# Optimization experiments

Measured on AMD Instinct MI355X. Metric: run time of the kernel, lower is better.

Reference implementation:

```python
import jax, jax.numpy as jnp
import numpy as np

H, C, PQ, PV, CZ, CS = 12, 16, 4, 8, 128, 384
W_C = (2.0 / (9.0 * PQ)) ** 0.5
INV_SQRT3 = 3.0 ** -0.5


def setup_inputs() -> dict:
    key = jax.random.key(0)
    ks = jax.random.split(key, 20)
    B, N = 2, 512
    s = jax.random.normal(ks[0], (B, N, CS), jnp.float32)
    z = jax.random.normal(ks[1], (B, N, N, CZ), jnp.float32)
    m = jax.random.normal(ks[2], (B, N, 3, 3), jnp.float32)
    rot, _ = jnp.linalg.qr(m)  # proper-ish rotations (orthonormal frames)
    trans = jax.random.normal(ks[3], (B, N, 3), jnp.float32)
    seq_mask = jnp.ones((B, N), jnp.float32)
    sc = 0.02
    params = {
        'Wq': jax.random.normal(ks[4], (CS, H * C)) * sc,
        'bq': jnp.zeros((H * C,)),
        'Wkv': jax.random.normal(ks[5], (CS, H * C * 2)) * sc,
        'bkv': jnp.zeros((H * C * 2,)),
        'Wb': jax.random.normal(ks[6], (CZ, H)) * sc,
        'bb': jnp.zeros((H,)),
        'Wqp': jax.random.normal(ks[7], (CS, 3 * PQ * H)) * sc,
        'bqp': jnp.zeros((3 * PQ * H,)),
        'Wkvp': jax.random.normal(ks[8], (CS, 3 * (PQ + PV) * H)) * sc,
        'bkvp': jnp.zeros((3 * (PQ + PV) * H,)),
        'gamma': jnp.zeros((H,)),
        'Wout': jax.random.normal(ks[9], ((CZ + C + PV * 4) * H, CS)) * sc,
        'bout': jnp.zeros((CS,)),
    }
    return dict(s=s, z=z, rot=rot, trans=trans, seq_mask=seq_mask, **params)


def reference(s, z, rot, trans, seq_mask, Wq, bq, Wkv, bkv, Wb, bb, Wqp, bqp, Wkvp, bkvp, gamma, Wout, bout):
    B, N, _ = s.shape
    # scalar q/k/v
    q = (s @ Wq + bq).reshape(B, N, H, C)
    kv = (s @ Wkv + bkv).reshape(B, N, H, 2 * C)
    k, v = kv[..., :C], kv[..., C:]
    qp = s @ Wqp + bqp                                   # (B,N,3*PQ*H)
    qp = jnp.stack(jnp.split(qp, 3, axis=-1), axis=-1)   # (B,N,PQ*H,3)
    qp = jnp.einsum('bixy,bipy->bipx', rot, qp) + trans[:, :, None, :]
    qp = qp.reshape(B, N, H, PQ, 3)
    # key/value points
    kvp = s @ Wkvp + bkvp
    kvp = jnp.stack(jnp.split(kvp, 3, axis=-1), axis=-1)  # (B,N,(PQ+PV)*H,3)
    kvp = jnp.einsum('bixy,bipy->bipx', rot, kvp) + trans[:, :, None, :]
    kvp = kvp.reshape(B, N, H, PQ + PV, 3)
    kp, vp = kvp[..., :PQ, :], kvp[..., PQ:, :]
    # attention logits: scalar term + pair bias + point-distance term
    bpair = (z @ Wb + bb).transpose(0, 3, 1, 2)          # (B,H,i,j)
    a = jnp.einsum('bihc,bjhc->bhij', q, k) * (3 * C) ** -0.5 + INV_SQRT3 * bpair
    d2 = jnp.sum((qp[:, :, None] - kp[:, None]) ** 2, axis=-1)   # (B,i,j,H,PQ)
    pa = -0.5 * jnp.sum(d2, axis=-1)                      # (B,i,j,H)
    head_w = jax.nn.softplus(gamma)
    pa = pa * (head_w * W_C * INV_SQRT3)
    a = a + pa.transpose(0, 3, 1, 2)
    mask_bias = 100000.0 * (seq_mask[:, :, None] * seq_mask[:, None, :] - 1.0)
    a = a + mask_bias[:, None, :, :]
    a = jax.nn.softmax(a, axis=-1)                        # (B,H,i,j)
    # outputs: scalar values, rotated points (inverse frame), pair features
    o = jnp.einsum('bhij,bjhc->bihc', a, v).reshape(B, N, H * C)
    op = jnp.einsum('bhij,bjhpx->bihpx', a, vp)           # (B,i,H,PV,3)
    op = jnp.einsum('biyx,bihpy->bihpx', rot, op - trans[:, :, None, None, :])  # R^T(p-t)
    onorm = jnp.maximum(jnp.sqrt(jnp.sum(op ** 2, axis=-1)), 1e-6).reshape(B, N, H * PV)
    op = op.reshape(B, N, H * PV, 3)
    opair = jnp.einsum('bhij,bijc->bihc', a, z).reshape(B, N, H * CZ)
    feat = jnp.concatenate([o, op[..., 0], op[..., 1], op[..., 2], onorm, opair], axis=-1)
    return feat @ Wout + bout
```

## Files before the change

### kernel.cpp

```cpp
#include <hip/hip_runtime.h>
#include <hip/hip_bf16.h>

constexpr int B = 2, N = 512, H = 12, C = 16, PQ = 4, PV = 8, CZ = 128, CS = 384;
constexpr int HC   = H * C;
constexpr int FEAT = (CZ + C + PV * 4) * H;
constexpr float QK_SCALE  = 0.14433756729740643f;
constexpr float INV_SQRT3 = 0.5773502691896258f;
constexpr float WC_IS3    = 0.13608276348795434f;

using f32x4 = __attribute__((ext_vector_type(4))) float;
using s16x8 = __attribute__((ext_vector_type(8))) short;

__device__ __forceinline__ short f2b(float f) {
    union { __hip_bfloat16 b; short s; } u;
    u.b = __float2bfloat16(f);
    return u.s;
}
__device__ __forceinline__ float b2f(short s) {
    union { short s; __hip_bfloat16 b; } u;
    u.s = s;
    return __bfloat162float(u.b);
}

constexpr int RPB = 2;

__global__ __launch_bounds__(256) void k_proj(
    const float* __restrict__ s, const float* __restrict__ rot, const float* __restrict__ trans,
    const float* __restrict__ Wq, const float* __restrict__ bq,
    const float* __restrict__ Wkv, const float* __restrict__ bkv,
    const float* __restrict__ Wqp, const float* __restrict__ bqp,
    const float* __restrict__ Wkvp, const float* __restrict__ bkvp,
    const float* __restrict__ gamma, const float* __restrict__ bb,
    const float* __restrict__ Wout,
    short* __restrict__ qcw, short* __restrict__ kkp,
    float* __restrict__ vw, float* __restrict__ vpw,
    short* __restrict__ pcw, float* __restrict__ auxw,
    short* __restrict__ WT)
{
    __shared__ float s_s[RPB][CS];
    __shared__ float rawqp_s[RPB][144];
    __shared__ float rawkvp_s[RPB][432];
    __shared__ float qrot_s[RPB][48][3];
    __shared__ float sq_s[RPB][48];
    __shared__ float R_s[RPB][9], T_s[RPB][3];
    const int t = threadIdx.x;
    const int bi0 = blockIdx.x * RPB;

    for (int idx = t; idx < RPB * CS / 4; idx += 256) {
        int r = idx / (CS / 4), k4 = idx % (CS / 4);
        ((float4*)s_s[r])[k4] = ((const float4*)(s + (size_t)(bi0 + r) * CS))[k4];
    }
    if (t < RPB * 9) R_s[t / 9][t % 9] = rot[bi0 * 9 + t];
    if (t < RPB * 3) T_s[t / 3][t % 3] = trans[bi0 * 3 + t];
    __syncthreads();

    for (int qd = t; qd < 288; qd += 256) {
        const int c = qd * 4;
        const float* Wp; int ldw; const float* bp;
        int seg;
        if (c < 192)      { Wp = Wq   + c;        ldw = 192; bp = bq + c;        seg = 0; }
        else if (c < 576) { Wp = Wkv  + (c - 192); ldw = 384; bp = bkv + (c - 192); seg = 1; }
        else if (c < 720) { Wp = Wqp  + (c - 576); ldw = 144; bp = bqp + (c - 576); seg = 2; }
        else              { Wp = Wkvp + (c - 720); ldw = 432; bp = bkvp + (c - 720); seg = 3; }
        float4 bv = *(const float4*)bp;
        float acc[RPB][4];
        #pragma unroll
        for (int r = 0; r < RPB; ++r) {
            acc[r][0] = bv.x; acc[r][1] = bv.y; acc[r][2] = bv.z; acc[r][3] = bv.w;
        }
        for (int k4 = 0; k4 < CS / 4; ++k4) {
            float4 sv[RPB];
            #pragma unroll
            for (int r = 0; r < RPB; ++r) sv[r] = *(const float4*)&s_s[r][k4 * 4];
            #pragma unroll
            for (int e = 0; e < 4; ++e) {
                float4 wv = *(const float4*)(Wp + (size_t)(k4 * 4 + e) * ldw);
                #pragma unroll
                for (int r = 0; r < RPB; ++r) {
                    float se = ((const float*)&sv[r])[e];
                    acc[r][0] += se * wv.x; acc[r][1] += se * wv.y;
                    acc[r][2] += se * wv.z; acc[r][3] += se * wv.w;
                }
            }
        }
        if (seg == 0) {
            #pragma unroll
            for (int r = 0; r < RPB; ++r) {
                short4 o = make_short4(f2b(QK_SCALE * acc[r][0]), f2b(QK_SCALE * acc[r][1]),
                                       f2b(QK_SCALE * acc[r][2]), f2b(QK_SCALE * acc[r][3]));
                *(short4*)&qcw[(size_t)(bi0 + r) * 192 + c] = o;
            }
        } else if (seg == 1) {
            int cc = c - 192, h = cc >> 5, w5 = cc & 31;
            if (w5 < 16) {
                #pragma unroll
                for (int r = 0; r < RPB; ++r) {
                    short4 o = make_short4(f2b(acc[r][0]), f2b(acc[r][1]),
                                           f2b(acc[r][2]), f2b(acc[r][3]));
                    *(short4*)&kkp[(size_t)(bi0 + r) * 384 + h * 16 + w5] = o;
                }
            } else {
                #pragma unroll
                for (int r = 0; r < RPB; ++r) {
                    int row = bi0 + r;
                    *(float4*)&vw[(size_t)row * 192 + h * 16 + (w5 - 16)] =
                        (float4){acc[r][0], acc[r][1], acc[r][2], acc[r][3]};
                }
            }
        } else if (seg == 2) {
            #pragma unroll
            for (int r = 0; r < RPB; ++r)
                *(float4*)&rawqp_s[r][c - 576] = (float4){acc[r][0], acc[r][1], acc[r][2], acc[r][3]};
        } else {
            #pragma unroll
            for (int r = 0; r < RPB; ++r)
                *(float4*)&rawkvp_s[r][c - 720] = (float4){acc[r][0], acc[r][1], acc[r][2], acc[r][3]};
        }
    }
    __syncthreads();

    for (int idx = t; idx < RPB * 48; idx += 256) {
        int r = idx / 48, p = idx % 48;
        float y0 = rawqp_s[r][p], y1 = rawqp_s[r][48 + p], y2 = rawqp_s[r][96 + p];
        #pragma unroll
        for (int x = 0; x < 3; ++x)
            qrot_s[r][p][x] = T_s[r][x] + R_s[r][x * 3] * y0 + R_s[r][x * 3 + 1] * y1 + R_s[r][x * 3 + 2] * y2;
    }
    for (int idx = t; idx < RPB * 144; idx += 256) {
        int r = idx / 144, p = idx % 144, h = p / 12, pp = p % 12;
        float y0 = rawkvp_s[r][p], y1 = rawkvp_s[r][144 + p], y2 = rawkvp_s[r][288 + p];
        float vals[3]; float ss = 0.0f;
        #pragma unroll
        for (int x = 0; x < 3; ++x) {
            float v = T_s[r][x] + R_s[r][x * 3] * y0 + R_s[r][x * 3 + 1] * y1 + R_s[r][x * 3 + 2] * y2;
            vals[x] = v; ss += v * v;
        }
        int row = bi0 + r;
        if (pp < PQ) {
            #pragma unroll
            for (int x = 0; x < 3; ++x)
                kkp[(size_t)row * 384 + 192 + h * 16 + pp * 3 + x] = f2b(vals[x]);
            sq_s[r][h * 4 + pp] = ss;
        } else {
            #pragma unroll
            for (int x = 0; x < 3; ++x)
                vpw[(size_t)row * 288 + h * 24 + (pp - PQ) * 3 + x] = vals[x];
        }
    }
    __syncthreads();

    if (t < RPB * 12) {
        int r = t / 12, h = t % 12, row = bi0 + r;
        float g = gamma[h];
        float sp = fmaxf(g, 0.0f) + log1pf(expf(-fabsf(g)));
        float pac = -0.5f * sp * WC_IS3;
        float kpsq = sq_s[r][h * 4] + sq_s[r][h * 4 + 1] + sq_s[r][h * 4 + 2] + sq_s[r][h * 4 + 3];
        kkp[(size_t)row * 384 + 192 + h * 16 + 12] = f2b(kpsq);
        kkp[(size_t)row * 384 + 192 + h * 16 + 13] = 0;
        kkp[(size_t)row * 384 + 192 + h * 16 + 14] = 0;
        kkp[(size_t)row * 384 + 192 + h * 16 + 15] = 0;
        float qpsq = 0.0f;
        #pragma unroll
        for (int pq = 0; pq < 4; ++pq)
            #pragma unroll
            for (int x = 0; x < 3; ++x) {
                float qv = qrot_s[r][h * 4 + pq][x];
                qpsq += qv * qv;
                pcw[(size_t)row * 192 + h * 16 + pq * 3 + x] = f2b(-2.0f * pac * qv);
            }
        pcw[(size_t)row * 192 + h * 16 + 12] = f2b(pac);
        pcw[(size_t)row * 192 + h * 16 + 13] = 0;
        pcw[(size_t)row * 192 + h * 16 + 14] = 0;
        pcw[(size_t)row * 192 + h * 16 + 15] = 0;
        auxw[(size_t)row * 16 + h] = INV_SQRT3 * bb[h] + pac * qpsq;
    }
    if (t >= RPB * 12 && t < RPB * 16) {
        int r = (t - RPB * 12) >> 2, hh = 12 + ((t - RPB * 12) & 3);
        auxw[(size_t)(bi0 + r) * 16 + hh] = 0.0f;
    }

    short* tileb = (short*)&s_s[0][0];
    for (int tile = blockIdx.x; tile < 66 * 12; tile += 512) {
        const int k0 = (tile % 66) * 32;
        const int c0 = (tile / 66) * 32;
        __syncthreads();
        {
            int r = t >> 3, c4 = (t & 7) * 4;
            float4 v = *(const float4*)&Wout[(size_t)(k0 + r) * CS + c0 + c4];
            tileb[(c4 + 0) * 33 + r] = f2b(v.x);
            tileb[(c4 + 1) * 33 + r] = f2b(v.y);
            tileb[(c4 + 2) * 33 + r] = f2b(v.z);
            tileb[(c4 + 3) * 33 + r] = f2b(v.w);
        }
        __syncthreads();
        {
            int rr = t >> 3, k4 = (t & 7) * 4;
            short4 o = make_short4(tileb[rr * 33 + k4], tileb[rr * 33 + k4 + 1],
                                   tileb[rr * 33 + k4 + 2], tileb[rr * 33 + k4 + 3]);
            *(short4*)&WT[(size_t)(c0 + rr) * FEAT + k0 + k4] = o;
        }
    }
}

constexpr int PLS = 520;
constexpr int BSEL = 56;

#define LOADZ(BUF, PTR)                                                  \
    {                                                                    \
        _Pragma("unroll")                                                \
        for (int k4 = 0; k4 < 4; ++k4) {                                 \
            BUF[k4 * 2]     = *(const float4*)((PTR) + k4 * 32);         \
            BUF[k4 * 2 + 1] = *(const float4*)((PTR) + k4 * 32 + 4);     \
        }                                                                \
    }

#define COMPUTE(BUF, JC, KPTR)                                                     \
    {                                                                              \
        s16x8 zf[4];                                                               \
        _Pragma("unroll")                                                          \
        for (int kk = 0; kk < 4; ++kk) {                                           \
            float4 u0 = BUF[kk * 2], u1 = BUF[kk * 2 + 1];                         \
            s16x8 f;                                                               \
            f[0] = f2b(u0.x); f[1] = f2b(u0.y); f[2] = f2b(u0.z); f[3] = f2b(u0.w);\
            f[4] = f2b(u1.x); f[5] = f2b(u1.y); f[6] = f2b(u1.z); f[7] = f2b(u1.w);\
            zf[kk] = f;                                                            \
        }                                                                          \
        f32x4 accA = (f32x4){0, 0, 0, 0}, accB = (f32x4){0, 0, 0, 0};              \
        f32x4 accC = (f32x4){0, 0, 0, 0}, accD = (f32x4){0, 0, 0, 0};              \
        _Pragma("unroll")                                                          \
        for (int kk = 0; kk < 4; ++kk) {                                           \
            s16x8 wb = *(const s16x8*)(bl + kk * 8);                               \
            accA = __builtin_amdgcn_mfma_f32_16x16x32_bf16(zf[kk], wb, accA, 0, 0, 0);\
        }                                                                          \
        s16x8 qselr = *(const s16x8*)(bl + 32);                                    \
        s16x8 pselr = *(const s16x8*)(bl + 40);                                    \
        _Pragma("unroll")                                                          \
        for (int kk = 0; kk < 4; ++kk) {                                           \
            s16x8 af = *(const s16x8*)((KPTR) + kk * 32);                          \
            s16x8 bsel = (kk == half) ? qselr : z8;                                \
            accB = __builtin_amdgcn_mfma_f32_16x16x32_bf16(af, bsel, accB, 0, 0, 0); \
        }                                                                          \
        _Pragma("unroll")                                                          \
        for (int kk = 4; kk < 8; ++kk) {                                           \
            s16x8 af = *(const s16x8*)((KPTR) + kk * 32);                          \
            s16x8 bsel;                                                            \
            if (kk < 6) bsel = (kk == half) ? qselr : z8;                          \
            else        bsel = ((kk - 6) == half) ? pselr : z8;                    \
            accC = __builtin_amdgcn_mfma_f32_16x16x32_bf16(af, bsel, accC, 0, 0, 0); \
        }                                                                          \
        _Pragma("unroll")                                                          \
        for (int kk = 8; kk < 12; ++kk) {                                          \
            s16x8 af = *(const s16x8*)((KPTR) + kk * 32);                          \
            s16x8 bsel = ((kk - 6) == half) ? pselr : z8;                          \
            accD = __builtin_amdgcn_mfma_f32_16x16x32_bf16(af, bsel, accD, 0, 0, 0); \
        }                                                                          \
        f32x4 acc = (accA + accB) + (accC + accD);                                 \
        float4 m4 = *(const float4*)(mkp + (JC) * 16);                             \
        float lo[4]; float cm = -INFINITY;                                         \
        _Pragma("unroll")                                                          \
        for (int r = 0; r < 4; ++r) {                                              \
            lo[r] = acc[r] + constH + 100000.0f * (mask_i * ((const float*)&m4)[r] - 1.0f); \
            cm = fmaxf(cm, lo[r]);                                                 \
        }                                                                          \
        cm = fmaxf(cm, __shfl_xor(cm, 16, 64));                                    \
        cm = fmaxf(cm, __shfl_xor(cm, 32, 64));                                    \
        float mnew = fmaxf(m_run, cm);                                             \
        float sc = __expf(m_run - mnew);                                           \
        m_run = mnew;                                                              \
        float p[4]; float ps = 0.0f;                                               \
        _Pragma("unroll")                                                          \
        for (int r = 0; r < 4; ++r) { p[r] = __expf(lo[r] - mnew); ps += p[r]; }   \
        ps += __shfl_xor(ps, 16, 64);                                              \
        ps += __shfl_xor(ps, 32, 64);                                              \
        l_run = l_run * sc + ps;                                                   \
        if (sc != 1.0f) {                                                          \
            for (int jj = lg * 4; jj < (JC) * 16; jj += 16) {                      \
                short* pr = &P_lds[m15 * PLS + jw + jj];                           \
                _Pragma("unroll")                                                  \
                for (int r = 0; r < 4; ++r) pr[r] = f2b(b2f(pr[r]) * sc);          \
            }                                                                      \
        }                                                                          \
        *(short4*)&P_lds[m15 * PLS + jw + (JC) * 16 + lg * 4] =                    \
            make_short4(f2b(p[0]), f2b(p[1]), f2b(p[2]), f2b(p[3]));               \
    }

__global__ __launch_bounds__(256) void k_attn2(
    const float* __restrict__ z, const float* __restrict__ rot, const float* __restrict__ trans,
    const float* __restrict__ seq_mask,
    const float* __restrict__ Wb,
    const short* __restrict__ qcw, const short* __restrict__ kkp,
    const short* __restrict__ pcw, const float* __restrict__ auxw,
    const float* __restrict__ vw, const float* __restrict__ vpw,
    short* __restrict__ featb)
{
    __shared__ short P_lds[16 * PLS];
    __shared__ __align__(16) char ovl[7680];
    short* bsel_lds = (short*)ovl;
    float* ored_s   = (float*)ovl;
    float* opred_s  = (float*)(ovl + 3072);
    float* op_f     = (float*)(ovl + 6528);
    __shared__ float ml_s[4][16], ll_s[4][16], M_s[16], Linv_s[16];
    __shared__ float R_s[9], T_s[3];

    const int t = threadIdx.x;
    const int w   = t >> 6;
    const int l   = t & 63;
    const int lg  = l >> 4;
    const int m15 = l & 15;
    const int bi  = blockIdx.x;
    const int b   = bi >> 9;
    const int i   = bi & (N - 1);

    if (t < 9) R_s[t] = rot[bi * 9 + t];
    if (t < 3) T_s[t] = trans[bi * 3 + t];

    const bool hv = (m15 < 12);
    const int hcl = hv ? m15 : 0;
    const int half = m15 >> 1;
    const float constH = auxw[(size_t)bi * 16 + m15];
    const float mask_i = seq_mask[bi];

    if (w == 0) {
        short* dst = &bsel_lds[l * BSEL];
        #pragma unroll
        for (int kk = 0; kk < 4; ++kk)
            #pragma unroll
            for (int e = 0; e < 8; ++e) {
                int c = kk * 32 + lg * 8 + e;
                dst[kk * 8 + e] = f2b(hv ? INV_SQRT3 * Wb[c * H + hcl] : 0.0f);
            }
        const bool selh = ((lg >> 1) == (m15 & 1));
        const s16x8 z8v = {0, 0, 0, 0, 0, 0, 0, 0};
        const short* qrow = qcw + (size_t)bi * 192 + hcl * 16;
        s16x8 qlo = *(const s16x8*)qrow;
        s16x8 qhi = *(const s16x8*)(qrow + 8);
        s16x8 q = (hv && selh) ? ((lg & 1) ? qhi : qlo) : z8v;
        const short* prow = pcw + (size_t)bi * 192 + hcl * 16;
        s16x8 plo = *(const s16x8*)prow;
        s16x8 phi = *(const s16x8*)(prow + 8);
        s16x8 p = (hv && selh) ? ((lg & 1) ? phi : plo) : z8v;
        *(s16x8*)(dst + 32) = q;
        *(s16x8*)(dst + 40) = p;
    }
    __syncthreads();

    float m_run = -INFINITY, l_run = 0.0f;

    const size_t zbase = ((size_t)b * N + i) * (size_t)(N * CZ);
    const int jw = w * 128;
    const float* zAp = z + zbase + (size_t)(jw + m15) * CZ + lg * 8;
    const short* kAp = kkp + (size_t)(b * N + jw + m15) * 384 + lg * 8;
    const float* mkp = seq_mask + b * N + jw + lg * 4;
    const short* bl = &bsel_lds[l * BSEL];
    const s16x8 z8 = {0, 0, 0, 0, 0, 0, 0, 0};

    float4 bufA[8], bufB[8];
    LOADZ(bufA, zAp);

    for (int jc2 = 0; jc2 < 8; jc2 += 2) {
        LOADZ(bufB, zAp + 16 * CZ);
        COMPUTE(bufA, jc2, kAp);
        kAp += 6144;
        {
            const float* nx = zAp + ((jc2 == 6) ? (16 * CZ) : (32 * CZ));
            LOADZ(bufA, nx);
        }
        COMPUTE(bufB, jc2 + 1, kAp);
        kAp += 6144;
        zAp += 32 * CZ;
    }

    if (lg == 0) { ml_s[w][m15] = m_run; ll_s[w][m15] = l_run; }
    __syncthreads();
    if (t < 16) {
        float M = ml_s[0][t];
        M = fmaxf(M, ml_s[1][t]); M = fmaxf(M, ml_s[2][t]); M = fmaxf(M, ml_s[3][t]);
        float Lt = 0.0f;
        #pragma unroll
        for (int ww = 0; ww < 4; ++ww) Lt += ll_s[ww][t] * __expf(ml_s[ww][t] - M);
        M_s[t] = M;
        Linv_s[t] = 1.0f / Lt;
    }
    __syncthreads();

    {
        const int h = t >> 4, j0t = (t & 15) * 32;
        const int wv = j0t >> 7;
        const float sS = __expf(ml_s[wv][h] - M_s[h]) * Linv_s[h];
        #pragma unroll
        for (int k = 0; k < 4; ++k) {
            s16x8 v = *(const s16x8*)&P_lds[h * PLS + j0t + k * 8];
            s16x8 o;
            #pragma unroll
            for (int e = 0; e < 8; ++e) o[e] = f2b(b2f(v[e]) * sS);
            *(s16x8*)&P_lds[h * PLS + j0t + k * 8] = o;
        }
    }
    __syncthreads();

    short* F = featb + (size_t)bi * FEAT;

    f32x4 oa0 = (f32x4){0, 0, 0, 0}, oa1 = (f32x4){0, 0, 0, 0};
    const int c0 = w * 32;
    #pragma unroll 4
    for (int kk = 0; kk < 16; ++kk) {
        s16x8 af = *(const s16x8*)&P_lds[m15 * PLS + kk * 32 + lg * 8];
        const float* zb = z + zbase + (size_t)(kk * 32 + lg * 8) * CZ + c0 + m15;
        s16x8 b0f, b1f;
        #pragma unroll
        for (int e = 0; e < 8; ++e) {
            b0f[e] = f2b(zb[(size_t)e * CZ]);
            b1f[e] = f2b(zb[(size_t)e * CZ + 16]);
        }
        oa0 = __builtin_amdgcn_mfma_f32_16x16x32_bf16(af, b0f, oa0, 0, 0, 0);
        oa1 = __builtin_amdgcn_mfma_f32_16x16x32_bf16(af, b1f, oa1, 0, 0, 0);
    }
    #pragma unroll
    for (int r = 0; r < 4; ++r) {
        int h = lg * 4 + r;
        if (h < 12) {
            F[576 + h * 128 + c0 + m15]      = f2b(oa0[r]);
            F[576 + h * 128 + c0 + 16 + m15] = f2b(oa1[r]);
        }
    }

    if (t < 192) {
        const int c4 = t % 48, jg = t / 48;
        const int h = c4 >> 2;
        const short* Pr = &P_lds[h * PLS + jg * 128];
        const float* vb = vw + ((size_t)b * N + jg * 128) * 192 + c4 * 4;
        f32x4 a = (f32x4){0, 0, 0, 0};
        #pragma unroll 2
        for (int q = 0; q < 16; ++q) {
            s16x8 pv = *(const s16x8*)(Pr + q * 8);
            #pragma unroll
            for (int e = 0; e < 8; ++e) {
                float4 v4 = *(const float4*)(vb + (size_t)(q * 8 + e) * 192);
                float pj = b2f(pv[e]);
                a[0] += pj * v4.x; a[1] += pj * v4.y; a[2] += pj * v4.z; a[3] += pj * v4.w;
            }
        }
        *(f32x4*)&ored_s[jg * 192 + c4 * 4] = a;
    }

    if (t < 216) {
        const int c4 = t % 72, jg = t / 72;
        const int h = c4 / 6;
        const int j0g = (jg == 0) ? 0 : (jg == 1 ? 176 : 352);
        const int nq = (jg == 2) ? 20 : 22;
        const short* Pr = &P_lds[h * PLS + j0g];
        const float* vb = vpw + ((size_t)b * N + j0g) * 288 + c4 * 4;
        f32x4 a = (f32x4){0, 0, 0, 0};
        #pragma unroll 2
        for (int q = 0; q < nq; ++q) {
            s16x8 pv = *(const s16x8*)(Pr + q * 8);
            #pragma unroll
            for (int e = 0; e < 8; ++e) {
                float4 v4 = *(const float4*)(vb + (size_t)(q * 8 + e) * 288);
                float pj = b2f(pv[e]);
                a[0] += pj * v4.x; a[1] += pj * v4.y; a[2] += pj * v4.z; a[3] += pj * v4.w;
            }
        }
        *(f32x4*)&opred_s[jg * 288 + c4 * 4] = a;
    }
    __syncthreads();

    if (t < 192)
        F[t] = f2b(ored_s[t] + ored_s[192 + t] + ored_s[384 + t] + ored_s[576 + t]);
    if (t < 72) {
        #pragma unroll
        for (int x = 0; x < 4; ++x) {
            int rv = t * 4 + x;
            op_f[rv] = opred_s[rv] + opred_s[288 + rv] + opred_s[576 + rv];
        }
    }
    __syncthreads();

    if (t < 96) {
        float o0 = op_f[t * 3 + 0] - T_s[0];
        float o1 = op_f[t * 3 + 1] - T_s[1];
        float o2 = op_f[t * 3 + 2] - T_s[2];
        float n2 = 0.0f;
        #pragma unroll
        for (int x = 0; x < 3; ++x) {
            float rx = R_s[0 * 3 + x] * o0 + R_s[1 * 3 + x] * o1 + R_s[2 * 3 + x] * o2;
            F[HC + 96 * x + t] = f2b(rx);
            n2 += rx * rx;
        }
        F[480 + t] = f2b(fmaxf(sqrtf(n2), 1e-6f));
    }
}

__global__ __launch_bounds__(256) void k_out(
    const short* __restrict__ featb, const short* __restrict__ WT,
    const float* __restrict__ bout, float* __restrict__ out)
{
    __shared__ short A_s[32 * 40];
    __shared__ short B_s[64 * 40];
    const int t = threadIdx.x;
    const int w   = t >> 6;
    const int l   = t & 63;
    const int lg  = l >> 4;
    const int m15 = l & 15;
    const int wm = w >> 1, wn = w & 1;
    const int bm = (blockIdx.x / 6) * 32;
    const int bn = (blockIdx.x % 6) * 64;

    f32x4 acc[2];
    acc[0] = (f32x4){0, 0, 0, 0};
    acc[1] = (f32x4){0, 0, 0, 0};

    const int sr = t >> 2;
    const int sk = (t & 3) * 8;

    s16x8 rA, rB;
    if (t < 128) rA = *(const s16x8*)&featb[(size_t)(bm + sr) * FEAT + sk];
    rB = *(const s16x8*)&WT[(size_t)(bn + sr) * FEAT + sk];

    for (int k0 = 0; k0 < FEAT; k0 += 32) {
        __syncthreads();
        if (t < 128) *(s16x8*)&A_s[sr * 40 + sk] = rA;
        *(s16x8*)&B_s[sr * 40 + sk] = rB;
        __syncthreads();

        const int kn = k0 + 32;
        if (kn < FEAT) {
            if (t < 128) rA = *(const s16x8*)&featb[(size_t)(bm + sr) * FEAT + kn + sk];
            rB = *(const s16x8*)&WT[(size_t)(bn + sr) * FEAT + kn + sk];
        }

        s16x8 af = *(const s16x8*)&A_s[(wm * 16 + m15) * 40 + lg * 8];
        #pragma unroll
        for (int sn = 0; sn < 2; ++sn) {
            s16x8 bf = *(const s16x8*)&B_s[(wn * 32 + sn * 16 + m15) * 40 + lg * 8];
            acc[sn] = __builtin_amdgcn_mfma_f32_16x16x32_bf16(af, bf, acc[sn], 0, 0, 0);
        }
    }

    #pragma unroll
    for (int sn = 0; sn < 2; ++sn) {
        int col = bn + wn * 32 + sn * 16 + m15;
        float bo = bout[col];
        #pragma unroll
        for (int r = 0; r < 4; ++r) {
            int row = bm + wm * 16 + lg * 4 + r;
            out[(size_t)row * CS + col] = acc[sn][r] + bo;
        }
    }
}

extern "C" void kernel_launch(void* const* d_in, const int* in_sizes, int n_in,
                              void* d_out, int out_size, void* d_ws, size_t ws_size,
                              hipStream_t stream)
{
    const float* s     = (const float*)d_in[0];
    const float* z     = (const float*)d_in[1];
    const float* rot   = (const float*)d_in[2];
    const float* trans = (const float*)d_in[3];
    const float* mask  = (const float*)d_in[4];
    const float* Wq    = (const float*)d_in[5];
    const float* bq    = (const float*)d_in[6];
    const float* Wkv   = (const float*)d_in[7];
    const float* bkv   = (const float*)d_in[8];
    const float* Wb    = (const float*)d_in[9];
    const float* bb    = (const float*)d_in[10];
    const float* Wqp   = (const float*)d_in[11];
    const float* bqp   = (const float*)d_in[12];
    const float* Wkvp  = (const float*)d_in[13];
    const float* bkvp  = (const float*)d_in[14];
    const float* gamma = (const float*)d_in[15];
    const float* Wout  = (const float*)d_in[16];
    const float* bout  = (const float*)d_in[17];

    char* wsb = (char*)d_ws;
    short* featb = (short*)wsb;
    float* vw    = (float*)(wsb + 4325376);
    float* vpw   = (float*)(wsb + 5111808);
    float* auxw  = (float*)(wsb + 6291456);
    short* qcw   = (short*)(wsb + 6356992);
    short* pcw   = (short*)(wsb + 6750208);
    short* kkp   = (short*)(wsb + 7143424);
    short* WT    = (short*)(wsb + 7929856);

    hipLaunchKernelGGL(k_proj, dim3(B * N / RPB), dim3(256), 0, stream,
                       s, rot, trans, Wq, bq, Wkv, bkv, Wqp, bqp, Wkvp, bkvp,
                       gamma, bb, Wout, qcw, kkp, vw, vpw, pcw, auxw, WT);
    hipLaunchKernelGGL(k_attn2, dim3(B * N), dim3(256), 0, stream,
                       z, rot, trans, mask, Wb, qcw, kkp, pcw, auxw, vw, vpw, featb);
    hipLaunchKernelGGL(k_out, dim3(96 * 2), dim3(256), 0, stream,
                       featb, WT, bout, (float*)d_out);
}
```

Measured before the change: 279.2 us.

## Swizzle K/point buffer into MFMA fragment tiles and retile output GEMM

The key/point buffer written by the projection kernel now uses a tiled layout (16 rows by 32 columns per tile, fragment-contiguous), so each lane in the attention kernel loads contiguous 8-element fragments with a fixed 512-element stride instead of strided row reads. The output GEMM moves from 32x64 to 32x32 tiles, doubling its grid to 384 blocks and using all 256 threads for staging, which adds parallelism at the cost of re-reading the feature rows more often. The projection inner loop also gets an unroll hint. The scattered writes of the new layout cost slightly more in the projection kernel.

```diff
diff --git a/kernel.cpp b/kernel.cpp
--- a/kernel.cpp
+++ b/kernel.cpp
@@ -20,6 +20,11 @@
     union { short s; __hip_bfloat16 b; } u;
     u.s = s;
     return __bfloat162float(u.b);
+}
+
+__device__ __forceinline__ size_t kkps_idx(int row, int col) {
+    return ((size_t)((row >> 4) * 12 + (col >> 5))) * 512
+         + (size_t)(((row & 15) << 2) + ((col & 31) >> 3)) * 8 + (col & 7);
 }
 
 constexpr int RPB = 2;
@@ -32,7 +37,7 @@
     const float* __restrict__ Wkvp, const float* __restrict__ bkvp,
     const float* __restrict__ gamma, const float* __restrict__ bb,
     const float* __restrict__ Wout,
-    short* __restrict__ qcw, short* __restrict__ kkp,
+    short* __restrict__ qcw, short* __restrict__ kkpS,
     float* __restrict__ vw, float* __restrict__ vpw,
     short* __restrict__ pcw, float* __restrict__ auxw,
     short* __restrict__ WT)
@@ -68,6 +73,7 @@
         for (int r = 0; r < RPB; ++r) {
             acc[r][0] = bv.x; acc[r][1] = bv.y; acc[r][2] = bv.z; acc[r][3] = bv.w;
         }
+        #pragma unroll 4
         for (int k4 = 0; k4 < CS / 4; ++k4) {
             float4 sv[RPB];
             #pragma unroll
@@ -93,11 +99,12 @@
         } else if (seg == 1) {
             int cc = c - 192, h = cc >> 5, w5 = cc & 31;
             if (w5 < 16) {
+                int col = h * 16 + w5;
                 #pragma unroll
                 for (int r = 0; r < RPB; ++r) {
                     short4 o = make_short4(f2b(acc[r][0]), f2b(acc[r][1]),
                                            f2b(acc[r][2]), f2b(acc[r][3]));
-                    *(short4*)&kkp[(size_t)(bi0 + r) * 384 + h * 16 + w5] = o;
+                    *(short4*)&kkpS[kkps_idx(bi0 + r, col)] = o;
                 }
             } else {
                 #pragma unroll
@@ -139,7 +146,7 @@
         if (pp < PQ) {
             #pragma unroll
             for (int x = 0; x < 3; ++x)
-                kkp[(size_t)row * 384 + 192 + h * 16 + pp * 3 + x] = f2b(vals[x]);
+                kkpS[kkps_idx(row, 192 + h * 16 + pp * 3 + x)] = f2b(vals[x]);
             sq_s[r][h * 4 + pp] = ss;
         } else {
             #pragma unroll
@@ -155,10 +162,10 @@
         float sp = fmaxf(g, 0.0f) + log1pf(expf(-fabsf(g)));
         float pac = -0.5f * sp * WC_IS3;
         float kpsq = sq_s[r][h * 4] + sq_s[r][h * 4 + 1] + sq_s[r][h * 4 + 2] + sq_s[r][h * 4 + 3];
-        kkp[(size_t)row * 384 + 192 + h * 16 + 12] = f2b(kpsq);
-        kkp[(size_t)row * 384 + 192 + h * 16 + 13] = 0;
-        kkp[(size_t)row * 384 + 192 + h * 16 + 14] = 0;
-        kkp[(size_t)row * 384 + 192 + h * 16 + 15] = 0;
+        kkpS[kkps_idx(row, 192 + h * 16 + 12)] = f2b(kpsq);
+        kkpS[kkps_idx(row, 192 + h * 16 + 13)] = 0;
+        kkpS[kkps_idx(row, 192 + h * 16 + 14)] = 0;
+        kkpS[kkps_idx(row, 192 + h * 16 + 15)] = 0;
         float qpsq = 0.0f;
         #pragma unroll
         for (int pq = 0; pq < 4; ++pq)
@@ -236,13 +243,13 @@
         s16x8 pselr = *(const s16x8*)(bl + 40);                                    \
         _Pragma("unroll")                                                          \
         for (int kk = 0; kk < 4; ++kk) {                                           \
-            s16x8 af = *(const s16x8*)((KPTR) + kk * 32);                          \
+            s16x8 af = *(const s16x8*)((KPTR) + kk * 512);                         \
             s16x8 bsel = (kk == half) ? qselr : z8;                                \
             accB = __builtin_amdgcn_mfma_f32_16x16x32_bf16(af, bsel, accB, 0, 0, 0); \
         }                                                                          \
         _Pragma("unroll")                                                          \
         for (int kk = 4; kk < 8; ++kk) {                                           \
-            s16x8 af = *(const s16x8*)((KPTR) + kk * 32);                          \
+            s16x8 af = *(const s16x8*)((KPTR) + kk * 512);                         \
             s16x8 bsel;                                                            \
             if (kk < 6) bsel = (kk == half) ? qselr : z8;                          \
             else        bsel = ((kk - 6) == half) ? pselr : z8;                    \
@@ -250,7 +257,7 @@
         }                                                                          \
         _Pragma("unroll")                                                          \
         for (int kk = 8; kk < 12; ++kk) {                                          \
-            s16x8 af = *(const s16x8*)((KPTR) + kk * 32);                          \
+            s16x8 af = *(const s16x8*)((KPTR) + kk * 512);                         \
             s16x8 bsel = ((kk - 6) == half) ? pselr : z8;                          \
             accD = __builtin_amdgcn_mfma_f32_16x16x32_bf16(af, bsel, accD, 0, 0, 0); \
         }                                                                          \
@@ -288,7 +295,7 @@
     const float* __restrict__ z, const float* __restrict__ rot, const float* __restrict__ trans,
     const float* __restrict__ seq_mask,
     const float* __restrict__ Wb,
-    const short* __restrict__ qcw, const short* __restrict__ kkp,
+    const short* __restrict__ qcw, const short* __restrict__ kkpS,
     const short* __restrict__ pcw, const float* __restrict__ auxw,
     const float* __restrict__ vw, const float* __restrict__ vpw,
     short* __restrict__ featb)
@@ -349,7 +356,8 @@
     const size_t zbase = ((size_t)b * N + i) * (size_t)(N * CZ);
     const int jw = w * 128;
     const float* zAp = z + zbase + (size_t)(jw + m15) * CZ + lg * 8;
-    const short* kAp = kkp + (size_t)(b * N + jw + m15) * 384 + lg * 8;
+    const short* kAp = kkpS + ((size_t)(b * 32 + (jw >> 4))) * 6144
+                            + (size_t)(m15 * 4 + lg) * 8;
     const float* mkp = seq_mask + b * N + jw + lg * 4;
     const short* bl = &bsel_lds[l * BSEL];
     const s16x8 z8 = {0, 0, 0, 0, 0, 0, 0, 0};
@@ -496,55 +504,49 @@
     const float* __restrict__ bout, float* __restrict__ out)
 {
     __shared__ short A_s[32 * 40];
-    __shared__ short B_s[64 * 40];
+    __shared__ short B_s[32 * 40];
     const int t = threadIdx.x;
     const int w   = t >> 6;
     const int l   = t & 63;
     const int lg  = l >> 4;
     const int m15 = l & 15;
     const int wm = w >> 1, wn = w & 1;
-    const int bm = (blockIdx.x / 6) * 32;
-    const int bn = (blockIdx.x % 6) * 64;
-
-    f32x4 acc[2];
-    acc[0] = (f32x4){0, 0, 0, 0};
-    acc[1] = (f32x4){0, 0, 0, 0};
-
-    const int sr = t >> 2;
+    const int bm = (blockIdx.x / 12) * 32;
+    const int bn = (blockIdx.x % 12) * 32;
+
+    f32x4 acc = (f32x4){0, 0, 0, 0};
+
+    const int sr = (t & 127) >> 2;
     const int sk = (t & 3) * 8;
 
-    s16x8 rA, rB;
-    if (t < 128) rA = *(const s16x8*)&featb[(size_t)(bm + sr) * FEAT + sk];
-    rB = *(const s16x8*)&WT[(size_t)(bn + sr) * FEAT + sk];
+    s16x8 rS;
+    if (t < 128) rS = *(const s16x8*)&featb[(size_t)(bm + sr) * FEAT + sk];
+    else         rS = *(const s16x8*)&WT[(size_t)(bn + sr) * FEAT + sk];
 
     for (int k0 = 0; k0 < FEAT; k0 += 32) {
         __syncthreads();
-        if (t < 128) *(s16x8*)&A_s[sr * 40 + sk] = rA;
-        *(s16x8*)&B_s[sr * 40 + sk] = rB;
+        if (t < 128) *(s16x8*)&A_s[sr * 40 + sk] = rS;
+        else         *(s16x8*)&B_s[sr * 40 + sk] = rS;
         __syncthreads();
 
         const int kn = k0 + 32;
         if (kn < FEAT) {
-            if (t < 128) rA = *(const s16x8*)&featb[(size_t)(bm + sr) * FEAT + kn + sk];
-            rB = *(const s16x8*)&WT[(size_t)(bn + sr) * FEAT + kn + sk];
+            if (t < 128) rS = *(const s16x8*)&featb[(size_t)(bm + sr) * FEAT + kn + sk];
+            else         rS = *(const s16x8*)&WT[(size_t)(bn + sr) * FEAT + kn + sk];
         }
 
         s16x8 af = *(const s16x8*)&A_s[(wm * 16 + m15) * 40 + lg * 8];
-        #pragma unroll
-        for (int sn = 0; sn < 2; ++sn) {
-            s16x8 bf = *(const s16x8*)&B_s[(wn * 32 + sn * 16 + m15) * 40 + lg * 8];
-            acc[sn] = __builtin_amdgcn_mfma_f32_16x16x32_bf16(af, bf, acc[sn], 0, 0, 0);
-        }
-    }
-
-    #pragma unroll
-    for (int sn = 0; sn < 2; ++sn) {
-        int col = bn + wn * 32 + sn * 16 + m15;
+        s16x8 bf = *(const s16x8*)&B_s[(wn * 16 + m15) * 40 + lg * 8];
+        acc = __builtin_amdgcn_mfma_f32_16x16x32_bf16(af, bf, acc, 0, 0, 0);
+    }
+
+    {
+        int col = bn + wn * 16 + m15;
         float bo = bout[col];
         #pragma unroll
         for (int r = 0; r < 4; ++r) {
             int row = bm + wm * 16 + lg * 4 + r;
-            out[(size_t)row * CS + col] = acc[sn][r] + bo;
+            out[(size_t)row * CS + col] = acc[r] + bo;
         }
     }
 }
@@ -579,14 +581,14 @@
     float* auxw  = (float*)(wsb + 6291456);
     short* qcw   = (short*)(wsb + 6356992);
     short* pcw   = (short*)(wsb + 6750208);
-    short* kkp   = (short*)(wsb + 7143424);
+    short* kkpS  = (short*)(wsb + 7143424);
     short* WT    = (short*)(wsb + 7929856);
 
     hipLaunchKernelGGL(k_proj, dim3(B * N / RPB), dim3(256), 0, stream,
                        s, rot, trans, Wq, bq, Wkv, bkv, Wqp, bqp, Wkvp, bkvp,
-                       gamma, bb, Wout, qcw, kkp, vw, vpw, pcw, auxw, WT);
+                       gamma, bb, Wout, qcw, kkpS, vw, vpw, pcw, auxw, WT);
     hipLaunchKernelGGL(k_attn2, dim3(B * N), dim3(256), 0, stream,
-                       z, rot, trans, mask, Wb, qcw, kkp, pcw, auxw, vw, vpw, featb);
-    hipLaunchKernelGGL(k_out, dim3(96 * 2), dim3(256), 0, stream,
+                       z, rot, trans, mask, Wb, qcw, kkpS, pcw, auxw, vw, vpw, featb);
+    hipLaunchKernelGGL(k_out, dim3(384), dim3(256), 0, stream,
                        featb, WT, bout, (float*)d_out);
 }
```

After: 426.8 us. +52.9%, slower.
